# Optimization experiments

Measured on AMD Instinct MI355X. Metric: run time of the kernel, lower is better.

Reference implementation:

```python
import jax, jax.numpy as jnp
import numpy as np

S, M, V, E, H = 128, 256, 32000, 1024, 512
PAD_ID = V - 1  # pad_id=-1 normalized to vocab-1


def setup_inputs() -> dict:
    key = jax.random.key(0)
    ks = jax.random.split(key, 9)
    F_lens = jax.random.randint(ks[0], (M,), 1, S + 1)
    tok = jax.random.randint(ks[1], (S, M), 1, PAD_ID)  # avoid 0 and PAD for valid tokens
    valid = jnp.arange(S)[:, None] < F_lens[None, :]
    F = jnp.where(valid, tok, PAD_ID)
    sc = 1.0 / np.sqrt(H)
    emb = jax.random.normal(ks[2], (V, E), jnp.float32) * 0.02
    emb = emb.at[PAD_ID].set(0.0)
    # PyTorch LSTM layout: gates [i, f, g, o]; bias_ih + bias_hh folded into one b.
    Wih0 = jax.random.uniform(ks[3], (2, 4 * H, E), jnp.float32, -sc, sc)
    Whh0 = jax.random.uniform(ks[4], (2, 4 * H, H), jnp.float32, -sc, sc)
    b0 = jax.random.uniform(ks[5], (2, 4 * H), jnp.float32, -sc, sc)
    Wih1 = jax.random.uniform(ks[6], (2, 4 * H, 2 * H), jnp.float32, -sc, sc)
    Whh1 = jax.random.uniform(ks[7], (2, 4 * H, H), jnp.float32, -sc, sc)
    b1 = jax.random.uniform(ks[8], (2, 4 * H), jnp.float32, -sc, sc)
    return dict(F=F, F_lens=F_lens, emb=emb, Wih0=Wih0, Whh0=Whh0, b0=b0,
                Wih1=Wih1, Whh1=Whh1, b1=b1)


def _run_lstm(x, mask, Wih, Whh, b):
    # x: [S, M, D], mask: [S, M] bool (update state only where valid, as packed seq does)
    m_ = x.shape[1]
    h_dim = Whh.shape[1]

    def step(carry, inp):
        h, c = carry
        xt, mt = inp
        g = xt @ Wih.T + h @ Whh.T + b
        i, f, gg, o = jnp.split(g, 4, axis=-1)
        c2 = jax.nn.sigmoid(f) * c + jax.nn.sigmoid(i) * jnp.tanh(gg)
        h2 = jax.nn.sigmoid(o) * jnp.tanh(c2)
        mt = mt[:, None]
        h2 = jnp.where(mt, h2, h)
        c2 = jnp.where(mt, c2, c)
        return (h2, c2), h2

    init = (jnp.zeros((m_, h_dim), x.dtype), jnp.zeros((m_, h_dim), x.dtype))
    _, hs = jax.lax.scan(step, init, (x, mask))
    return hs


def _bilstm_layer(x, mask, idx, Wih, Whh, b):
    # forward direction
    hf = _run_lstm(x, mask, Wih[0], Whh[0], b[0])
    # backward direction: per-sequence reverse within valid length (packed semantics)
    xr = jnp.take_along_axis(x, idx[:, :, None], axis=0)
    hb = _run_lstm(xr, mask, Wih[1], Whh[1], b[1])
    hb = jnp.take_along_axis(hb, idx[:, :, None], axis=0)  # idx is an involution on valid t
    return jnp.concatenate([hf, hb], axis=-1)


def reference(F, F_lens, emb, Wih0, Whh0, b0, Wih1, Whh1, b1):
    s_ = F.shape[0]
    t = jnp.arange(s_)[:, None]
    valid = t < F_lens[None, :]                      # [S, M]
    idx = jnp.where(valid, F_lens[None, :] - 1 - t, t)
    # embedding with padding_idx zeroing (matches nn.Embedding padding_idx + explicit loop)
    x = jnp.where((F != PAD_ID)[:, :, None], emb[F], 0.0)
    h1 = _bilstm_layer(x, valid, idx, Wih0, Whh0, b0)
    h2 = _bilstm_layer(h1, valid, idx, Wih1, Whh1, b1)
    # pad_packed_sequence(padding_value=h_pad=0) + final F==0 masking loop, fused
    keep = valid & (F != 0)
    return jnp.where(keep[:, :, None], h2, 0.0)
```

## Files before the change

### kernel.cpp

```cpp
#include <hip/hip_runtime.h>
#include <hip/hip_bf16.h>

#define S_LEN 128
#define M_B   256
#define E_DIM 1024
#define H_DIM 512
#define G4    2048
#define N_ROWS (S_LEN*M_B)
#define KD    1024

typedef __bf16 bf16_t;
typedef __bf16 bf16x8 __attribute__((ext_vector_type(8)));
typedef float  f32x4  __attribute__((ext_vector_type(4)));
typedef int    i32x4  __attribute__((ext_vector_type(4)));

#define AS1(p) ((const __attribute__((address_space(1))) void*)(p))
#define AS3(p) ((__attribute__((address_space(3))) void*)(p))

__device__ __forceinline__ float sigm(float x)     { return 1.f / (1.f + __expf(-x)); }
__device__ __forceinline__ float tanhfast(float x) { return 2.f / (1.f + __expf(-2.f * x)) - 1.f; }

__device__ __forceinline__ void store_h_dev(bf16_t* p, bf16_t v) {
    unsigned int w = (unsigned int)__builtin_bit_cast(unsigned short, v);
    asm volatile("global_store_short %0, %1, off sc0 sc1" :: "v"(p), "v"(w) : "memory");
}
__device__ __forceinline__ bf16x8 load_h_dev(const bf16_t* p) {
    i32x4 r;
    asm volatile("global_load_dwordx4 %0, %1, off sc0 sc1" : "=v"(r) : "v"(p) : "memory");
    return __builtin_bit_cast(bf16x8, r);
}
__device__ __forceinline__ float load_f32_async(const float* p) {
    float r;
    asm volatile("global_load_dword %0, %1, off" : "=v"(r) : "v"(p) : "memory");
    return r;
}

__global__ __launch_bounds__(256)
void permute_weights_kernel(const float* __restrict__ Wih, const float* __restrict__ Whh,
                            const float* __restrict__ b,
                            bf16_t* __restrict__ Wihp, bf16_t* __restrict__ Whhp,
                            float* __restrict__ bp)
{
    int bid = blockIdx.x;
    int d  = bid >> 11;
    int jp = bid & 2047;
    int q = jp >> 6, r = jp & 63;
    int gate = r >> 4, u16 = r & 15;
    int j = gate * H_DIM + q * 16 + u16;

    const float* s_ih = Wih + ((size_t)d * G4 + j) * E_DIM;
    bf16_t*      d_ih = Wihp + ((size_t)d * G4 + jp) * E_DIM;
    for (int e = threadIdx.x; e < E_DIM; e += 256) d_ih[e] = (bf16_t)s_ih[e];

    const float* s_hh = Whh + ((size_t)d * G4 + j) * H_DIM;
    bf16_t*      d_hh = Whhp + ((size_t)d * G4 + jp) * H_DIM;
    for (int k = threadIdx.x; k < H_DIM; k += 256) d_hh[k] = (bf16_t)s_hh[k];

    if (threadIdx.x == 0) bp[d * G4 + jp] = b[d * G4 + j];
}

__global__ __launch_bounds__(256)
void embed_kernel(const int* __restrict__ F, const float* __restrict__ emb,
                  bf16_t* __restrict__ X)
{
    int n   = blockIdx.x;
    int tok = F[n];
    const float4* src = (const float4*)(emb + (size_t)tok * E_DIM);
    bf16_t*       dst = X + (size_t)n * E_DIM;
    for (int i = threadIdx.x; i < E_DIM / 4; i += 256) {
        float4 v = src[i];
        dst[i * 4 + 0] = (bf16_t)v.x;
        dst[i * 4 + 1] = (bf16_t)v.y;
        dst[i * 4 + 2] = (bf16_t)v.z;
        dst[i * 4 + 3] = (bf16_t)v.w;
    }
}

__global__ __launch_bounds__(256)
void rowmap_kernel(const int* __restrict__ F_lens, int* __restrict__ srcrow)
{
    int n = blockIdx.x * 256 + threadIdx.x;
    int t = n >> 8, m = n & 255;
    int L = F_lens[m];
    int st = (t < L) ? (L - 1 - t) : t;
    srcrow[n] = st * M_B + m;
}

#define BM 128
#define BN 128
#define BK 32

__global__ __launch_bounds__(256)
void gemm_pre_kernel(const bf16_t* __restrict__ A,
                     const bf16_t* __restrict__ Wp,
                     const float* __restrict__ bp,
                     const int* __restrict__ srcrow,
                     float* __restrict__ PREc,
                     int rowbase, int TCR)
{
    const int nwg = gridDim.x;
    const int qx  = nwg >> 3;
    const int orig = blockIdx.x;
    const int wg   = (orig & 7) * qx + (orig >> 3);
    const int MT   = TCR / BM;
    const int n_t  = wg & 15;
    const int m_t  = (wg >> 4) % MT;
    const int d    = wg / (16 * MT);

    const int n0   = n_t * BN;
    const int mloc = m_t * BM;
    const int tid  = threadIdx.x;
    const int lane = tid & 63, wave = tid >> 6;
    const int wm = wave >> 1, wn = wave & 1;
    const int fr = lane & 15, fq = lane >> 4;

    __shared__ __attribute__((aligned(16))) bf16_t At[BM * BK];
    __shared__ __attribute__((aligned(16))) bf16_t Bt[BN * BK];

    const int r0 = tid >> 2;
    const int k8 = (tid & 3) * 8;
    const int n_0 = rowbase + mloc + r0;
    const int n_1 = n_0 + 64;
    const size_t srow0 = (d == 1) ? (size_t)srcrow[n_0] : (size_t)n_0;
    const size_t srow1 = (d == 1) ? (size_t)srcrow[n_1] : (size_t)n_1;
    const bf16_t* Ar0 = A + srow0 * KD + k8;
    const bf16_t* Ar1 = A + srow1 * KD + k8;
    const bf16_t* Br0 = Wp + ((size_t)d * G4 + n0 + r0) * KD + k8;
    const bf16_t* Br1 = Br0 + (size_t)64 * KD;

    f32x4 acc[4][4];
#pragma unroll
    for (int i = 0; i < 4; ++i)
#pragma unroll
        for (int j = 0; j < 4; ++j) { f32x4 z = {0.f, 0.f, 0.f, 0.f}; acc[i][j] = z; }

    for (int kt = 0; kt < KD; kt += BK) {
        __builtin_amdgcn_global_load_lds(AS1(Ar0 + kt), AS3(&At[(wave * 64) * 8]),       16, 0, 0);
        __builtin_amdgcn_global_load_lds(AS1(Ar1 + kt), AS3(&At[(256 + wave * 64) * 8]), 16, 0, 0);
        __builtin_amdgcn_global_load_lds(AS1(Br0 + kt), AS3(&Bt[(wave * 64) * 8]),       16, 0, 0);
        __builtin_amdgcn_global_load_lds(AS1(Br1 + kt), AS3(&Bt[(256 + wave * 64) * 8]), 16, 0, 0);
        __syncthreads();
        bf16x8 af[4], bff[4];
#pragma unroll
        for (int i = 0; i < 4; ++i) {
            af[i]  = *(const bf16x8*)&At[(wm * 64 + i * 16 + fr) * BK + fq * 8];
            bff[i] = *(const bf16x8*)&Bt[(wn * 64 + i * 16 + fr) * BK + fq * 8];
        }
#pragma unroll
        for (int i = 0; i < 4; ++i)
#pragma unroll
            for (int j = 0; j < 4; ++j)
                acc[i][j] = __builtin_amdgcn_mfma_f32_16x16x32_bf16(af[i], bff[j], acc[i][j], 0, 0, 0);
        __syncthreads();
    }

    const int cb = n0 + wn * 64 + fr;
#pragma unroll
    for (int mi = 0; mi < 4; ++mi) {
#pragma unroll
        for (int rr = 0; rr < 4; ++rr) {
            int r = mloc + wm * 64 + mi * 16 + fq * 4 + rr;
            float* prow = PREc + ((size_t)d * TCR + r) * G4;
#pragma unroll
            for (int ni = 0; ni < 4; ++ni) {
                int col = cb + ni * 16;
                prow[col] = acc[mi][ni][rr] + bp[d * G4 + col];
            }
        }
    }
}

__global__ __launch_bounds__(256)
void lstm_chunk_kernel(const bf16_t* __restrict__ Whhp,
                       const float* __restrict__ PREc,
                       const int* __restrict__ F_lens,
                       float* __restrict__ cfb,
                       bf16_t* __restrict__ hbA,
                       bf16_t* __restrict__ hbB,
                       bf16_t* __restrict__ H1,
                       float* __restrict__ OUT,
                       unsigned int* __restrict__ ctr,
                       int t0, int TC, int TCR, int mode, int s_base)
{
    const int d  = blockIdx.z;
    const int bx = blockIdx.x;
    const int m0 = blockIdx.y * 64;
    const int tid = threadIdx.x;
    const int lane = tid & 63, wave = tid >> 6;
    const int fr = lane & 15, fq = lane >> 4;
    const int gslot = ((blockIdx.y << 1) | d) * 16;

    __shared__ __attribute__((aligned(16))) bf16_t Bt[64 * 512];

    const bf16_t* Bg = Whhp + ((size_t)d * G4 + bx * 64) * H_DIM;
#pragma unroll
    for (int it = 0; it < 16; ++it) {
        int c   = it * 256 + tid;
        int row = c >> 6, ck = c & 63;
        int cks = ck ^ (row & 7);
        __builtin_amdgcn_global_load_lds(AS1(Bg + (size_t)row * H_DIM + cks * 8),
                                         AS3(&Bt[(it * 256 + wave * 64) * 8]), 16, 0, 0);
    }

    const int mrow  = m0 + wave * 16 + fr;
    const int u     = bx * 16 + fr;
    const int cbcol = bx * 64 + fr;
    int mm[4], LL[4], sidx[4];
    float c_own[4], h_own[4];
    const float* pbase[4];
#pragma unroll
    for (int rr = 0; rr < 4; ++rr) {
        mm[rr]   = m0 + wave * 16 + fq * 4 + rr;
        LL[rr]   = F_lens[mm[rr]];
        sidx[rr] = (d * M_B + mm[rr]) * H_DIM + u;
        c_own[rr]= cfb[sidx[rr]];
        pbase[rr]= PREc + ((size_t)d * TCR + mm[rr]) * G4 + cbcol;
    }
    {
        const bf16_t* hin0 = (t0 & 1) ? hbB : hbA;
#pragma unroll
        for (int rr = 0; rr < 4; ++rr) h_own[rr] = (float)hin0[sidx[rr]];
    }

    float pv[4][4];
#pragma unroll
    for (int rr = 0; rr < 4; ++rr) {
#pragma unroll
        for (int g = 0; g < 4; ++g)
            pv[rr][g] = load_f32_async(pbase[rr] + g * 16);
    }

    __syncthreads();

    for (int tt = 0; tt < TC; ++tt) {
        const int t = t0 + tt;
        const bf16_t* hin  = (t & 1) ? hbB : hbA;
        bf16_t*       hout = (t & 1) ? hbA : hbB;

        const bf16_t* Arow = hin + ((size_t)d * M_B + mrow) * H_DIM + fq * 8;
        bf16x8 af[16];
#pragma unroll
        for (int ks = 0; ks < 16; ++ks)
            af[ks] = load_h_dev(Arow + ks * 32);
        asm volatile("s_waitcnt vmcnt(0)" ::: "memory");
        __builtin_amdgcn_sched_barrier(0);

        f32x4 acc[4];
#pragma unroll
        for (int j = 0; j < 4; ++j) { f32x4 z = {0.f, 0.f, 0.f, 0.f}; acc[j] = z; }

#pragma unroll
        for (int ks = 0; ks < 16; ++ks) {
#pragma unroll
            for (int j = 0; j < 4; ++j) {
                int rb = j * 16 + fr;
                int ck = (ks * 4 + fq) ^ (rb & 7);
                bf16x8 bf = *(const bf16x8*)&Bt[rb * 512 + ck * 8];
                acc[j] = __builtin_amdgcn_mfma_f32_16x16x32_bf16(af[ks], bf, acc[j], 0, 0, 0);
            }
        }

#pragma unroll
        for (int rr = 0; rr < 4; ++rr) {
            bool mt = (t < LL[rr]);
            float gi = acc[0][rr] + pv[rr][0];
            float gf = acc[1][rr] + pv[rr][1];
            float gg = acc[2][rr] + pv[rr][2];
            float go = acc[3][rr] + pv[rr][3];
            float c2 = sigm(gf) * c_own[rr] + sigm(gi) * tanhfast(gg);
            float h2 = sigm(go) * tanhfast(c2);
            if (!mt) { c2 = c_own[rr]; h2 = h_own[rr]; }
            c_own[rr] = c2;
            h_own[rr] = h2;
            store_h_dev(&hout[sidx[rr]], (bf16_t)h2);
        }
        asm volatile("s_waitcnt vmcnt(0)" ::: "memory");
        __syncthreads();
        if (tid == 0)
            __hip_atomic_fetch_add(&ctr[gslot], 1u, __ATOMIC_RELAXED, __HIP_MEMORY_SCOPE_AGENT);

#pragma unroll
        for (int rr = 0; rr < 4; ++rr) {
            bool mt = (t < LL[rr]);
            int trow = (d == 0 || !mt) ? t : (LL[rr] - 1 - t);
            size_t orow = (size_t)trow * M_B + mm[rr];
            if (mode == 0) H1[orow * 1024 + d * H_DIM + u] = (bf16_t)h_own[rr];
            else           OUT[orow * 1024 + d * H_DIM + u] = mt ? h_own[rr] : 0.f;
        }
        float pvn[4][4];
        if (tt + 1 < TC) {
#pragma unroll
            for (int rr = 0; rr < 4; ++rr) {
                const float* prow = pbase[rr] + (size_t)(tt + 1) * ((size_t)M_B * G4);
#pragma unroll
                for (int g = 0; g < 4; ++g)
                    pvn[rr][g] = load_f32_async(prow + g * 16);
            }
        }

        if (tid == 0) {
            unsigned int tgt = (unsigned int)(s_base + tt + 1) * 32u;
            while (__hip_atomic_load(&ctr[gslot], __ATOMIC_RELAXED, __HIP_MEMORY_SCOPE_AGENT) < tgt)
                __builtin_amdgcn_s_sleep(2);
        }
        __syncthreads();

        if (tt + 1 < TC) {
#pragma unroll
            for (int rr = 0; rr < 4; ++rr)
#pragma unroll
                for (int g = 0; g < 4; ++g)
                    pv[rr][g] = pvn[rr][g];
        }
    }

#pragma unroll
    for (int rr = 0; rr < 4; ++rr) cfb[sidx[rr]] = c_own[rr];
}

extern "C" void kernel_launch(void* const* d_in, const int* in_sizes, int n_in,
                              void* d_out, int out_size, void* d_ws, size_t ws_size,
                              hipStream_t stream)
{
    const int*   F      = (const int*)d_in[0];
    const int*   F_lens = (const int*)d_in[1];
    const float* emb    = (const float*)d_in[2];
    const float* Wih0   = (const float*)d_in[3];
    const float* Whh0   = (const float*)d_in[4];
    const float* b0     = (const float*)d_in[5];
    const float* Wih1   = (const float*)d_in[6];
    const float* Whh1   = (const float*)d_in[7];
    const float* b1     = (const float*)d_in[8];
    float* OUT = (float*)d_out;

    char* p = (char*)d_ws;
    auto alloc = [&](size_t bytes) { char* q = p; p += (bytes + 255) & ~(size_t)255; return (void*)q; };
    bf16_t* X0    = (bf16_t*)alloc((size_t)N_ROWS * E_DIM * 2);
    bf16_t* H1    = (bf16_t*)alloc((size_t)N_ROWS * 1024 * 2);
    bf16_t* Wih0p = (bf16_t*)alloc((size_t)2 * G4 * E_DIM * 2);
    bf16_t* Whh0p = (bf16_t*)alloc((size_t)2 * G4 * H_DIM * 2);
    bf16_t* Wih1p = (bf16_t*)alloc((size_t)2 * G4 * E_DIM * 2);
    bf16_t* Whh1p = (bf16_t*)alloc((size_t)2 * G4 * H_DIM * 2);
    float*  b0p   = (float*)alloc((size_t)2 * G4 * 4);
    float*  b1p   = (float*)alloc((size_t)2 * G4 * 4);
    int*    srcrow= (int*)alloc((size_t)N_ROWS * 4);
    bf16_t* hbA   = (bf16_t*)alloc((size_t)2 * M_B * H_DIM * 2);
    bf16_t* hbB   = (bf16_t*)alloc((size_t)2 * M_B * H_DIM * 2);
    float*  cfb   = (float*)alloc((size_t)2 * M_B * H_DIM * 4);
    unsigned int* ctr = (unsigned int*)alloc(512);
    size_t base_used = (size_t)(p - (char*)d_ws);

    int TC = 0;
    const int tcs[8] = {128, 64, 32, 16, 8, 4, 2, 1};
    for (int i = 0; i < 8; ++i) {
        size_t need = base_used + (size_t)2 * tcs[i] * M_B * G4 * 4;
        if (need <= ws_size) { TC = tcs[i]; break; }
    }
    if (TC == 0) return;
    float* PREc = (float*)p;
    const int TCR = TC * M_B;

    hipMemsetAsync(ctr, 0, 512, stream);
    permute_weights_kernel<<<dim3(2 * G4), 256, 0, stream>>>(Wih0, Whh0, b0, Wih0p, Whh0p, b0p);
    permute_weights_kernel<<<dim3(2 * G4), 256, 0, stream>>>(Wih1, Whh1, b1, Wih1p, Whh1p, b1p);
    embed_kernel<<<dim3(N_ROWS), 256, 0, stream>>>(F, emb, X0);
    rowmap_kernel<<<dim3(N_ROWS / 256), 256, 0, stream>>>(F_lens, srcrow);

    for (int layer = 0; layer < 2; ++layer) {
        const bf16_t* Xin  = layer ? H1 : X0;
        const bf16_t* Wihp = layer ? Wih1p : Wih0p;
        const bf16_t* Whhp = layer ? Whh1p : Whh0p;
        const float*  bp   = layer ? b1p : b0p;

        hipMemsetAsync(hbA, 0, (size_t)2 * M_B * H_DIM * 2, stream);
        hipMemsetAsync(cfb, 0, (size_t)2 * M_B * H_DIM * 4, stream);

        for (int c = 0; c < S_LEN / TC; ++c) {
            gemm_pre_kernel<<<dim3(2 * (TCR / BM) * 16), 256, 0, stream>>>(
                Xin, Wihp, bp, srcrow, PREc, c * TCR, TCR);

            lstm_chunk_kernel<<<dim3(32, 4, 2), dim3(256), 0, stream>>>(
                Whhp, PREc, F_lens, cfb, hbA, hbB, H1, OUT, ctr,
                c * TC, TC, TCR, layer, layer * S_LEN + c * TC);
        }
    }
}
```

Baseline: 2.552 ms.

## Double GEMM K-tile with XOR-swizzled LDS and merge setup kernels

The input-projection GEMM now stages a 64-wide K tile per iteration instead of 32, and applies an XOR swizzle to the LDS column layout to avoid bank conflicts on the fragment reads. This halves the number of barrier pairs per GEMM and does two MFMA K-steps per sync, at the cost of double the LDS footprint and more registers for the fragments. Separately, the two weight-permute launches are merged into one, and the row-map computation is folded into the embedding kernel, which removes two small kernel launches.

```diff
diff --git a/kernel.cpp b/kernel.cpp
--- a/kernel.cpp
+++ b/kernel.cpp
@@ -36,18 +36,29 @@
 }
 
 __global__ __launch_bounds__(256)
-void permute_weights_kernel(const float* __restrict__ Wih, const float* __restrict__ Whh,
-                            const float* __restrict__ b,
-                            bf16_t* __restrict__ Wihp, bf16_t* __restrict__ Whhp,
-                            float* __restrict__ bp)
+void permute_all_kernel(const float* __restrict__ Wih0, const float* __restrict__ Whh0,
+                        const float* __restrict__ b0,
+                        const float* __restrict__ Wih1, const float* __restrict__ Whh1,
+                        const float* __restrict__ b1,
+                        bf16_t* __restrict__ Wih0p, bf16_t* __restrict__ Whh0p,
+                        bf16_t* __restrict__ Wih1p, bf16_t* __restrict__ Whh1p,
+                        float* __restrict__ b0p, float* __restrict__ b1p)
 {
     int bid = blockIdx.x;
-    int d  = bid >> 11;
-    int jp = bid & 2047;
+    int lay = bid >> 12;
+    int d   = (bid >> 11) & 1;
+    int jp  = bid & 2047;
     int q = jp >> 6, r = jp & 63;
     int gate = r >> 4, u16 = r & 15;
     int j = gate * H_DIM + q * 16 + u16;
 
+    const float* Wih = lay ? Wih1 : Wih0;
+    const float* Whh = lay ? Whh1 : Whh0;
+    const float* b   = lay ? b1 : b0;
+    bf16_t* Wihp = lay ? Wih1p : Wih0p;
+    bf16_t* Whhp = lay ? Whh1p : Whh0p;
+    float*  bp   = lay ? b1p : b0p;
+
     const float* s_ih = Wih + ((size_t)d * G4 + j) * E_DIM;
     bf16_t*      d_ih = Wihp + ((size_t)d * G4 + jp) * E_DIM;
     for (int e = threadIdx.x; e < E_DIM; e += 256) d_ih[e] = (bf16_t)s_ih[e];
@@ -61,7 +72,8 @@
 
 __global__ __launch_bounds__(256)
 void embed_kernel(const int* __restrict__ F, const float* __restrict__ emb,
-                  bf16_t* __restrict__ X)
+                  const int* __restrict__ F_lens,
+                  bf16_t* __restrict__ X, int* __restrict__ srcrow)
 {
     int n   = blockIdx.x;
     int tok = F[n];
@@ -74,21 +86,17 @@
         dst[i * 4 + 2] = (bf16_t)v.z;
         dst[i * 4 + 3] = (bf16_t)v.w;
     }
-}
-
-__global__ __launch_bounds__(256)
-void rowmap_kernel(const int* __restrict__ F_lens, int* __restrict__ srcrow)
-{
-    int n = blockIdx.x * 256 + threadIdx.x;
-    int t = n >> 8, m = n & 255;
-    int L = F_lens[m];
-    int st = (t < L) ? (L - 1 - t) : t;
-    srcrow[n] = st * M_B + m;
+    if (threadIdx.x == 0) {
+        int t = n >> 8, m = n & 255;
+        int L = F_lens[m];
+        int st = (t < L) ? (L - 1 - t) : t;
+        srcrow[n] = st * M_B + m;
+    }
 }
 
 #define BM 128
 #define BN 128
-#define BK 32
+#define BKG 64
 
 __global__ __launch_bounds__(256)
 void gemm_pre_kernel(const bf16_t* __restrict__ A,
@@ -114,19 +122,19 @@
     const int wm = wave >> 1, wn = wave & 1;
     const int fr = lane & 15, fq = lane >> 4;
 
-    __shared__ __attribute__((aligned(16))) bf16_t At[BM * BK];
-    __shared__ __attribute__((aligned(16))) bf16_t Bt[BN * BK];
-
-    const int r0 = tid >> 2;
-    const int k8 = (tid & 3) * 8;
-    const int n_0 = rowbase + mloc + r0;
-    const int n_1 = n_0 + 64;
-    const size_t srow0 = (d == 1) ? (size_t)srcrow[n_0] : (size_t)n_0;
-    const size_t srow1 = (d == 1) ? (size_t)srcrow[n_1] : (size_t)n_1;
-    const bf16_t* Ar0 = A + srow0 * KD + k8;
-    const bf16_t* Ar1 = A + srow1 * KD + k8;
-    const bf16_t* Br0 = Wp + ((size_t)d * G4 + n0 + r0) * KD + k8;
-    const bf16_t* Br1 = Br0 + (size_t)64 * KD;
+    __shared__ __attribute__((aligned(16))) bf16_t At[BM * BKG];
+    __shared__ __attribute__((aligned(16))) bf16_t Bt[BN * BKG];
+
+    const int rA = tid >> 3;
+    const int co = (((tid & 7) ^ (rA & 7)) << 3);
+    size_t srowA[4];
+    const bf16_t* Bp[4];
+#pragma unroll
+    for (int it = 0; it < 4; ++it) {
+        int nn = rowbase + mloc + rA + it * 32;
+        srowA[it] = (d == 1) ? (size_t)srcrow[nn] : (size_t)nn;
+        Bp[it] = Wp + ((size_t)d * G4 + n0 + rA + it * 32) * KD + co;
+    }
 
     f32x4 acc[4][4];
 #pragma unroll
@@ -134,23 +142,37 @@
 #pragma unroll
         for (int j = 0; j < 4; ++j) { f32x4 z = {0.f, 0.f, 0.f, 0.f}; acc[i][j] = z; }
 
-    for (int kt = 0; kt < KD; kt += BK) {
-        __builtin_amdgcn_global_load_lds(AS1(Ar0 + kt), AS3(&At[(wave * 64) * 8]),       16, 0, 0);
-        __builtin_amdgcn_global_load_lds(AS1(Ar1 + kt), AS3(&At[(256 + wave * 64) * 8]), 16, 0, 0);
-        __builtin_amdgcn_global_load_lds(AS1(Br0 + kt), AS3(&Bt[(wave * 64) * 8]),       16, 0, 0);
-        __builtin_amdgcn_global_load_lds(AS1(Br1 + kt), AS3(&Bt[(256 + wave * 64) * 8]), 16, 0, 0);
+    for (int kt = 0; kt < KD; kt += BKG) {
+#pragma unroll
+        for (int it = 0; it < 4; ++it)
+            __builtin_amdgcn_global_load_lds(AS1(A + srowA[it] * KD + kt + co),
+                                             AS3(&At[(it * 256 + wave * 64) * 8]), 16, 0, 0);
+#pragma unroll
+        for (int it = 0; it < 4; ++it)
+            __builtin_amdgcn_global_load_lds(AS1(Bp[it] + kt),
+                                             AS3(&Bt[(it * 256 + wave * 64) * 8]), 16, 0, 0);
         __syncthreads();
-        bf16x8 af[4], bff[4];
-#pragma unroll
-        for (int i = 0; i < 4; ++i) {
-            af[i]  = *(const bf16x8*)&At[(wm * 64 + i * 16 + fr) * BK + fq * 8];
-            bff[i] = *(const bf16x8*)&Bt[(wn * 64 + i * 16 + fr) * BK + fq * 8];
-        }
-#pragma unroll
-        for (int i = 0; i < 4; ++i)
-#pragma unroll
-            for (int j = 0; j < 4; ++j)
-                acc[i][j] = __builtin_amdgcn_mfma_f32_16x16x32_bf16(af[i], bff[j], acc[i][j], 0, 0, 0);
+
+        bf16x8 af[2][4], bff[2][4];
+#pragma unroll
+        for (int ks = 0; ks < 2; ++ks) {
+#pragma unroll
+            for (int i = 0; i < 4; ++i) {
+                int ra = wm * 64 + i * 16 + fr;
+                int ca = (ks * 4 + fq) ^ (ra & 7);
+                af[ks][i] = *(const bf16x8*)&At[ra * BKG + ca * 8];
+                int rb = wn * 64 + i * 16 + fr;
+                int cbk = (ks * 4 + fq) ^ (rb & 7);
+                bff[ks][i] = *(const bf16x8*)&Bt[rb * BKG + cbk * 8];
+            }
+        }
+#pragma unroll
+        for (int ks = 0; ks < 2; ++ks)
+#pragma unroll
+            for (int i = 0; i < 4; ++i)
+#pragma unroll
+                for (int j = 0; j < 4; ++j)
+                    acc[i][j] = __builtin_amdgcn_mfma_f32_16x16x32_bf16(af[ks][i], bff[ks][j], acc[i][j], 0, 0, 0);
         __syncthreads();
     }
 
@@ -361,10 +383,9 @@
     const int TCR = TC * M_B;
 
     hipMemsetAsync(ctr, 0, 512, stream);
-    permute_weights_kernel<<<dim3(2 * G4), 256, 0, stream>>>(Wih0, Whh0, b0, Wih0p, Whh0p, b0p);
-    permute_weights_kernel<<<dim3(2 * G4), 256, 0, stream>>>(Wih1, Whh1, b1, Wih1p, Whh1p, b1p);
-    embed_kernel<<<dim3(N_ROWS), 256, 0, stream>>>(F, emb, X0);
-    rowmap_kernel<<<dim3(N_ROWS / 256), 256, 0, stream>>>(F_lens, srcrow);
+    permute_all_kernel<<<dim3(2 * 2 * G4), 256, 0, stream>>>(
+        Wih0, Whh0, b0, Wih1, Whh1, b1, Wih0p, Whh0p, Wih1p, Whh1p, b0p, b1p);
+    embed_kernel<<<dim3(N_ROWS), 256, 0, stream>>>(F, emb, F_lens, X0, srcrow);
 
     for (int layer = 0; layer < 2; ++layer) {
         const bf16_t* Xin  = layer ? H1 : X0;
```

Measured after the change: 2.463 ms. 1.04x faster.
